# Optimization experiments

Measured on AMD Instinct MI355X. Metric: run time of the kernel, lower is better.

## Reference

```python
import jax, jax.numpy as jnp
import numpy as np

D_MODEL = 512
D_AUX = 64
B, E = 8, 2048


def setup_inputs() -> dict:
    key = jax.random.key(0)
    ks = jax.random.split(key, 12)
    x = jax.random.normal(ks[0], (B, E, D_MODEL), dtype=jnp.float32)
    query_aux = jax.random.normal(ks[1], (B, E, D_AUX), dtype=jnp.float32)
    key_aux = jax.random.normal(ks[2], (B, E, D_AUX), dtype=jnp.float32)
    adjacency_mask = jax.random.randint(ks[3], (B, E, E), 0, 2, dtype=jnp.int32)
    merge_coefficients = jax.random.uniform(ks[4], (B, E, E), dtype=jnp.float32)
    # learned parameters of IrregularityAwareAttention (nn.Linear weights stored
    # as (out, in) in torch; we keep (in, out) for x @ W)
    s = 1.0 / np.sqrt(D_MODEL)
    Wq = jax.random.uniform(ks[5], (D_MODEL, D_MODEL), minval=-s, maxval=s, dtype=jnp.float32)
    bq = jax.random.uniform(ks[6], (D_MODEL,), minval=-s, maxval=s, dtype=jnp.float32)
    Wk = jax.random.uniform(ks[7], (D_MODEL, D_MODEL), minval=-s, maxval=s, dtype=jnp.float32)
    bk = jax.random.uniform(ks[8], (D_MODEL,), minval=-s, maxval=s, dtype=jnp.float32)
    Wv = jax.random.uniform(ks[9], (D_MODEL, D_MODEL), minval=-s, maxval=s, dtype=jnp.float32)
    bv = jax.random.uniform(ks[10], (D_MODEL,), minval=-s, maxval=s, dtype=jnp.float32)
    threshold = jnp.float32(0.5)
    return {
        "x": x, "query_aux": query_aux, "key_aux": key_aux,
        "adjacency_mask": adjacency_mask, "merge_coefficients": merge_coefficients,
        "Wq": Wq, "bq": bq, "Wk": Wk, "bk": bk, "Wv": Wv, "bv": bv,
        "threshold": threshold,
    }


def reference(x, query_aux, key_aux, adjacency_mask, merge_coefficients,
              Wq, bq, Wk, bk, Wv, bv, threshold):
    d_model = x.shape[-1]
    scale = jnp.asarray(d_model, x.dtype) ** 0.5
    q = x @ Wq + bq                      # (B, E, D)
    k = x @ Wk + bk
    v = x @ Wv + bv
    scores = jnp.einsum("bed,bfd->bef", q, k) / scale   # (B, E, E)

    aux_scale = jnp.asarray(key_aux.shape[-1], x.dtype) ** 0.5
    scores_aux = jnp.einsum("bed,bfd->bef", query_aux, key_aux) / aux_scale

    non_zero_mask = scores_aux != 0
    positive_mask = scores > threshold
    merge_mask = positive_mask & non_zero_mask
    blended = (1.0 - merge_coefficients) * scores + merge_coefficients * scores_aux
    scores = jnp.where(merge_mask, blended, scores)

    mask_value = jnp.finfo(scores.dtype).min
    scores = jnp.where(adjacency_mask == 0, mask_value, scores)

    attn = jax.nn.softmax(scores, axis=-1)
    return jnp.einsum("bef,bfd->bed", attn, v)
```

## Files before the change

### kernel.cpp

```cpp
#include <hip/hip_runtime.h>

#define E2 2048
#define DM 512

typedef __attribute__((ext_vector_type(8))) _Float16 half8;
typedef __attribute__((ext_vector_type(4))) _Float16 half4;
typedef __attribute__((ext_vector_type(8))) short short8;
typedef __attribute__((ext_vector_type(4))) short shortx4;
typedef __attribute__((ext_vector_type(4))) float floatx4;

__device__ __forceinline__ void stage_tile(const _Float16* __restrict__ g, int stride,
                                           _Float16* lds, int tid) {
  const int r0 = tid >> 2;
  const int cs = ((tid & 3) ^ (r0 & 3)) * 8;
  const int wbase = (tid >> 6) * 512;
#pragma unroll
  for (int h = 0; h < 2; ++h) {
    const _Float16* gp = g + (size_t)(h * 64 + r0) * stride + cs;
    _Float16* lp = lds + h * 2048 + wbase;
    __builtin_amdgcn_global_load_lds(
        (const __attribute__((address_space(1))) unsigned int*)gp,
        (__attribute__((address_space(3))) unsigned int*)lp, 16, 0, 0);
  }
}

__device__ __forceinline__ void stage_tile8(const _Float16* __restrict__ g, int stride,
                                            _Float16* lds, int tid) {
  const int r0 = tid >> 2;
  const int cs = ((tid & 3) ^ (r0 & 3)) * 8;
  const int wbase = (tid >> 6) * 512;
  const _Float16* gp = g + (size_t)r0 * stride + cs;
  __builtin_amdgcn_global_load_lds(
      (const __attribute__((address_space(1))) unsigned int*)gp,
      (__attribute__((address_space(3))) unsigned int*)(lds + wbase), 16, 0, 0);
}

__device__ __forceinline__ void mfma16(const _Float16* As, const _Float16* Bs,
                                       floatx4 acc[4][4], int wm, int wn, int lane) {
  const int m16 = lane & 15, quad = lane >> 4;
  const int sq = (quad ^ (m16 & 3)) * 8;
  half8 a[4];
#pragma unroll
  for (int i = 0; i < 4; ++i)
    a[i] = *(const half8*)(As + (wm * 64 + i * 16 + m16) * 32 + sq);
#pragma unroll
  for (int j = 0; j < 4; ++j) {
    const half8 b = *(const half8*)(Bs + (wn * 64 + j * 16 + m16) * 32 + sq);
#pragma unroll
    for (int i = 0; i < 4; ++i)
      acc[i][j] = __builtin_amdgcn_mfma_f32_16x16x32_f16(a[i], b, acc[i][j], 0, 0, 0);
  }
}

__device__ __forceinline__ void mfma8(const _Float16* As, const _Float16* Bs,
                                      floatx4 acc[4][2], int wm, int wn, int lane) {
  const int m16 = lane & 15, quad = lane >> 4;
  const int sq = (quad ^ (m16 & 3)) * 8;
  half8 a[4];
#pragma unroll
  for (int i = 0; i < 4; ++i)
    a[i] = *(const half8*)(As + (wm * 64 + i * 16 + m16) * 32 + sq);
#pragma unroll
  for (int j = 0; j < 2; ++j) {
    const half8 b = *(const half8*)(Bs + (wn * 32 + j * 16 + m16) * 32 + sq);
#pragma unroll
    for (int i = 0; i < 4; ++i)
      acc[i][j] = __builtin_amdgcn_mfma_f32_16x16x32_f16(a[i], b, acc[i][j], 0, 0, 0);
  }
}

__device__ __forceinline__ void mfma24(const _Float16* Ah, const _Float16* Al,
                                       const _Float16* Bh, const _Float16* Bl,
                                       floatx4 acc[4][2], int wm, int wn, int lane) {
  const int m16 = lane & 15, quad = lane >> 4;
  const int sq = (quad ^ (m16 & 3)) * 8;
  half8 ah[4], al[4];
#pragma unroll
  for (int i = 0; i < 4; ++i) {
    const int off = (wm * 64 + i * 16 + m16) * 32 + sq;
    ah[i] = *(const half8*)(Ah + off);
    al[i] = *(const half8*)(Al + off);
  }
#pragma unroll
  for (int j = 0; j < 2; ++j) {
    const int off = (wn * 32 + j * 16 + m16) * 32 + sq;
    const half8 bh = *(const half8*)(Bh + off);
    const half8 bl = *(const half8*)(Bl + off);
#pragma unroll
    for (int i = 0; i < 4; ++i) {
      acc[i][j] = __builtin_amdgcn_mfma_f32_16x16x32_f16(ah[i], bh, acc[i][j], 0, 0, 0);
      acc[i][j] = __builtin_amdgcn_mfma_f32_16x16x32_f16(al[i], bh, acc[i][j], 0, 0, 0);
      acc[i][j] = __builtin_amdgcn_mfma_f32_16x16x32_f16(ah[i], bl, acc[i][j], 0, 0, 0);
    }
  }
}

__global__ void split_conv_k(const float* __restrict__ src, _Float16* __restrict__ hi,
                             _Float16* __restrict__ lo, float scale, int n8) {
  int i = blockIdx.x * blockDim.x + threadIdx.x;
  const int stride = gridDim.x * blockDim.x;
  const float4* s4 = (const float4*)src;
  for (; i < n8; i += stride) {
    const float4 u = s4[2 * i], v = s4[2 * i + 1];
    const float g[8] = {u.x, u.y, u.z, u.w, v.x, v.y, v.z, v.w};
    half8 h, l;
#pragma unroll
    for (int t = 0; t < 8; ++t) {
      const float gv = g[t] * scale;
      const _Float16 hv = (_Float16)gv;
      h[t] = hv;
      l[t] = (_Float16)(gv - (float)hv);
    }
    ((half8*)hi)[i] = h;
    ((half8*)lo)[i] = l;
  }
}

__global__ void conv_k(const float* __restrict__ src, _Float16* __restrict__ dst, int n8) {
  int i = blockIdx.x * blockDim.x + threadIdx.x;
  const int stride = gridDim.x * blockDim.x;
  const float4* s4 = (const float4*)src;
  for (; i < n8; i += stride) {
    const float4 u = s4[2 * i], v = s4[2 * i + 1];
    const float g[8] = {u.x, u.y, u.z, u.w, v.x, v.y, v.z, v.w};
    half8 h;
#pragma unroll
    for (int t = 0; t < 8; ++t) h[t] = (_Float16)g[t];
    ((half8*)dst)[i] = h;
  }
}

__global__ void transw_k(const float* __restrict__ Wq, const float* __restrict__ Wk,
                         const float* __restrict__ Wv, _Float16* __restrict__ Wth,
                         _Float16* __restrict__ Wtl) {
  const int z = blockIdx.z;
  const float* W = (z == 0) ? Wq : (z == 1) ? Wk : Wv;
  __shared__ float t[32][33];
  const int n0 = blockIdx.x * 32, k0 = blockIdx.y * 32;
  const int tx = threadIdx.x, ty = threadIdx.y;
#pragma unroll
  for (int i = 0; i < 32; i += 8) t[ty + i][tx] = W[(size_t)(k0 + ty + i) * DM + n0 + tx];
  __syncthreads();
  const size_t zb = (size_t)z * DM * DM;
#pragma unroll
  for (int i = 0; i < 32; i += 8) {
    const float g = t[tx][ty + i] * 64.0f;
    const _Float16 h = (_Float16)g;
    const size_t o = zb + (size_t)(n0 + ty + i) * DM + (k0 + tx);
    Wth[o] = h;
    Wtl[o] = (_Float16)(g - (float)h);
  }
}

__global__ __launch_bounds__(512, 4) void qkv_k(
    const _Float16* __restrict__ xh, const _Float16* __restrict__ xl,
    const _Float16* __restrict__ Wth, const _Float16* __restrict__ Wtl,
    const float* __restrict__ bqp, const float* __restrict__ bkp,
    const float* __restrict__ bvp,
    _Float16* __restrict__ qh, _Float16* __restrict__ ql,
    _Float16* __restrict__ kh, _Float16* __restrict__ kl,
    _Float16* __restrict__ vT) {
  __shared__ _Float16 Ah[2][4096], Al[2][4096], Bh[2][4096], Bl[2][4096];
  const int tid = threadIdx.x, lane = tid & 63, wv = tid >> 6;
  const int wm = wv >> 2, wn = wv & 3;
  const int bm = blockIdx.x, bn = blockIdx.y, z = blockIdx.z;
  const bool split = (z < 2);
  const _Float16* Ash = xh + (size_t)bm * 128 * DM;
  const _Float16* Asl = xl + (size_t)bm * 128 * DM;
  const _Float16* Bsh = Wth + ((size_t)z * DM + bn * 128) * DM;
  const _Float16* Bsl = Wtl + ((size_t)z * DM + bn * 128) * DM;
  floatx4 acc[4][2];
  const floatx4 z4 = {0.f, 0.f, 0.f, 0.f};
#pragma unroll
  for (int i = 0; i < 4; ++i)
#pragma unroll
    for (int j = 0; j < 2; ++j) acc[i][j] = z4;

  stage_tile8(Ash, DM, Ah[0], tid);
  stage_tile8(Bsh, DM, Bh[0], tid);
  if (split) { stage_tile8(Asl, DM, Al[0], tid); stage_tile8(Bsl, DM, Bl[0], tid); }
  __syncthreads();
  for (int kt = 0; kt < 16; ++kt) {
    const int cur = kt & 1, nxt = cur ^ 1;
    if (kt < 15) {
      const int ko = (kt + 1) * 32;
      stage_tile8(Ash + ko, DM, Ah[nxt], tid);
      stage_tile8(Bsh + ko, DM, Bh[nxt], tid);
      if (split) { stage_tile8(Asl + ko, DM, Al[nxt], tid); stage_tile8(Bsl + ko, DM, Bl[nxt], tid); }
    }
    if (split) mfma24(Ah[cur], Al[cur], Bh[cur], Bl[cur], acc, wm, wn, lane);
    else       mfma8(Ah[cur], Bh[cur], acc, wm, wn, lane);
    __syncthreads();
  }
  const int m16 = lane & 15, quad = lane >> 4;
  const float* bias = (z == 0) ? bqp : (z == 1) ? bkp : bvp;
  if (split) {
    _Float16* oh = (z == 0) ? qh : kh;
    _Float16* ol = (z == 0) ? ql : kl;
#pragma unroll
    for (int j = 0; j < 2; ++j) {
      const int n = bn * 128 + wn * 32 + j * 16 + m16;
      const float bb = bias[n];
#pragma unroll
      for (int i = 0; i < 4; ++i) {
        const int m = bm * 128 + wm * 64 + i * 16 + quad * 4;
#pragma unroll
        for (int r = 0; r < 4; ++r) {
          const float val = acc[i][j][r] * (1.0f / 256.0f) + bb;
          const float v8 = val * 8.0f;
          const _Float16 h = (_Float16)v8;
          const _Float16 l = (_Float16)(v8 - (float)h);
          const size_t o = (size_t)(m + r) * DM + n;
          oh[o] = h; ol[o] = l;
        }
      }
    }
  } else {
#pragma unroll
    for (int j = 0; j < 2; ++j) {
      const int n = bn * 128 + wn * 32 + j * 16 + m16;
      const float bb = bias[n];
#pragma unroll
      for (int i = 0; i < 4; ++i) {
        const int m = bm * 128 + wm * 64 + i * 16 + quad * 4;
        const int bidx = m >> 11, e0 = m & 2047;
        half4 pk;
#pragma unroll
        for (int r = 0; r < 4; ++r)
          pk[r] = (_Float16)(acc[i][j][r] * (1.0f / 256.0f) + bb);
        *(half4*)(vT + ((size_t)bidx * DM + n) * E2 + e0) = pk;
      }
    }
  }
}

__global__ __launch_bounds__(512, 4) void scores_k(
    const _Float16* __restrict__ qh, const _Float16* __restrict__ ql,
    const _Float16* __restrict__ kh, const _Float16* __restrict__ kl,
    const _Float16* __restrict__ qah, const _Float16* __restrict__ kah,
    const float* __restrict__ mc,
    const float* __restrict__ thrp, unsigned short* __restrict__ sc) {
  __shared__ _Float16 S[32768];
  _Float16* const AhB = S;
  _Float16* const AlB = S + 8192;
  _Float16* const BhB = S + 16384;
  _Float16* const BlB = S + 24576;
  const int tid = threadIdx.x, lane = tid & 63, wv = tid >> 6;
  const int wm = wv >> 2, wn = wv & 3;
  const int bf = blockIdx.x, be = blockIdx.y, b = blockIdx.z;
  const _Float16* Ash = qh + ((size_t)b * E2 + be * 128) * DM;
  const _Float16* Asl = ql + ((size_t)b * E2 + be * 128) * DM;
  const _Float16* Bsh = kh + ((size_t)b * E2 + bf * 128) * DM;
  const _Float16* Bsl = kl + ((size_t)b * E2 + bf * 128) * DM;
  floatx4 accm[4][2];
  const floatx4 z4 = {0.f, 0.f, 0.f, 0.f};
#pragma unroll
  for (int i = 0; i < 4; ++i)
#pragma unroll
    for (int j = 0; j < 2; ++j) accm[i][j] = z4;

  stage_tile8(Ash, DM, AhB, tid);
  stage_tile8(Bsh, DM, BhB, tid);
  stage_tile8(Asl, DM, AlB, tid);
  stage_tile8(Bsl, DM, BlB, tid);
  __syncthreads();
  for (int kt = 0; kt < 16; ++kt) {
    const int cur = kt & 1, nxt = cur ^ 1;
    if (kt < 15) {
      const int ko = (kt + 1) * 32;
      stage_tile8(Ash + ko, DM, AhB + nxt * 4096, tid);
      stage_tile8(Bsh + ko, DM, BhB + nxt * 4096, tid);
      stage_tile8(Asl + ko, DM, AlB + nxt * 4096, tid);
      stage_tile8(Bsl + ko, DM, BlB + nxt * 4096, tid);
    }
    mfma24(AhB + cur * 4096, AlB + cur * 4096, BhB + cur * 4096, BlB + cur * 4096,
           accm, wm, wn, lane);
    __syncthreads();
  }
  floatx4 acca[4][2];
#pragma unroll
  for (int i = 0; i < 4; ++i)
#pragma unroll
    for (int j = 0; j < 2; ++j) acca[i][j] = z4;
  const _Float16* A2 = qah + ((size_t)b * E2 + be * 128) * 64;
  const _Float16* B2 = kah + ((size_t)b * E2 + bf * 128) * 64;
  stage_tile8(A2, 64, AhB, tid);
  stage_tile8(B2, 64, BhB, tid);
  stage_tile8(A2 + 32, 64, AhB + 4096, tid);
  stage_tile8(B2 + 32, 64, BhB + 4096, tid);
  __syncthreads();
  mfma8(AhB, BhB, acca, wm, wn, lane);
  mfma8(AhB + 4096, BhB + 4096, acca, wm, wn, lane);

  float* const sL = (float*)S;
  _Float16* const saL = S + 16896;
  const float thr = *thrp;
  const int m16 = lane & 15, quad = lane >> 4;
  const size_t rowbase0 = (size_t)b * E2 + be * 128;
#pragma unroll
  for (int h = 0; h < 2; ++h) {
    __syncthreads();
    if (wm == h) {
#pragma unroll
      for (int j = 0; j < 2; ++j) {
        const int cl = wn * 32 + j * 16 + m16;
#pragma unroll
        for (int i = 0; i < 4; ++i) {
#pragma unroll
          for (int r = 0; r < 4; ++r) {
            const int rl = i * 16 + quad * 4 + r;
            sL[rl * 132 + cl] = accm[i][j][r] * (0.015625f * 0.044194173824159216f);
            saL[rl * 132 + cl] = (_Float16)(acca[i][j][r] * 0.125f);
          }
        }
      }
    }
    __syncthreads();
#pragma unroll
    for (int g = 0; g < 4; ++g) {
      const int tf = g * 2048 + tid * 4;
      const int rl = tf >> 7, cl = tf & 127;
      const size_t idx = (rowbase0 + h * 64 + rl) * E2 + bf * 128 + cl;
      const float4 c4 = *(const float4*)(mc + idx);
      const float4 s4v = *(const float4*)(sL + rl * 132 + cl);
      const half4 sa4 = *(const half4*)(saL + rl * 132 + cl);
      const float ss[4] = {s4v.x, s4v.y, s4v.z, s4v.w};
      const float cc[4] = {c4.x, c4.y, c4.z, c4.w};
      shortx4 o;
#pragma unroll
      for (int t = 0; t < 4; ++t) {
        float s = ss[t];
        const float sa = (float)sa4[t];
        if (sa != 0.0f && s > thr) s = (1.0f - cc[t]) * s + cc[t] * sa;
        union { _Float16 hh; unsigned short u; } u;
        u.hh = (_Float16)s;
        o[t] = (short)u.u;
      }
      *(shortx4*)(sc + idx) = o;
    }
  }
}

__global__ __launch_bounds__(256) void smax_k(unsigned short* __restrict__ sc,
                                              const int* __restrict__ adj) {
  const size_t row = blockIdx.x;
  unsigned short* p = sc + row * E2;
  const int* arow = adj + row * E2;
  const int tid = threadIdx.x, lane = tid & 63, wv = tid >> 6;
  const short8 raw = *(const short8*)(p + tid * 8);
  const int4 a0 = *(const int4*)(arow + tid * 8);
  const int4 a1 = *(const int4*)(arow + tid * 8 + 4);
  const int aa[8] = {a0.x, a0.y, a0.z, a0.w, a1.x, a1.y, a1.z, a1.w};
  float f[8];
#pragma unroll
  for (int t = 0; t < 8; ++t) {
    union { _Float16 h; short s; } u; u.s = raw[t];
    f[t] = aa[t] ? (float)u.h : -65504.0f;
  }
  float mx = f[0];
#pragma unroll
  for (int t = 1; t < 8; ++t) mx = fmaxf(mx, f[t]);
#pragma unroll
  for (int o = 32; o > 0; o >>= 1) mx = fmaxf(mx, __shfl_xor(mx, o, 64));
  __shared__ float red[8];
  if (lane == 0) red[wv] = mx;
  __syncthreads();
  mx = fmaxf(fmaxf(red[0], red[1]), fmaxf(red[2], red[3]));
  float ef[8], sum = 0.f;
#pragma unroll
  for (int t = 0; t < 8; ++t) { ef[t] = __expf(f[t] - mx); sum += ef[t]; }
#pragma unroll
  for (int o = 32; o > 0; o >>= 1) sum += __shfl_xor(sum, o, 64);
  if (lane == 0) red[4 + wv] = sum;
  __syncthreads();
  sum = (red[4] + red[5]) + (red[6] + red[7]);
  const float inv = 1.0f / sum;
  short8 ov;
#pragma unroll
  for (int t = 0; t < 8; ++t) {
    union { _Float16 h; short s; } u;
    u.h = (_Float16)(ef[t] * inv);
    ov[t] = u.s;
  }
  *(short8*)(p + tid * 8) = ov;
}

__global__ __launch_bounds__(256, 2) void pv_k(
    const _Float16* __restrict__ at, const _Float16* __restrict__ vT,
    float* __restrict__ out) {
  __shared__ _Float16 As[2][4096], Bs[2][4096];
  const int tid = threadIdx.x, lane = tid & 63, wv = tid >> 6;
  const int wm = wv >> 1, wn = wv & 1;
  const int bd = blockIdx.x, be = blockIdx.y, b = blockIdx.z;
  const _Float16* Asrc = at + ((size_t)b * E2 + be * 128) * E2;
  const _Float16* Bsrc = vT + ((size_t)b * DM + bd * 128) * E2;
  floatx4 acc[4][4];
  const floatx4 z4 = {0.f, 0.f, 0.f, 0.f};
#pragma unroll
  for (int i = 0; i < 4; ++i)
#pragma unroll
    for (int j = 0; j < 4; ++j) acc[i][j] = z4;
  stage_tile(Asrc, E2, As[0], tid);
  stage_tile(Bsrc, E2, Bs[0], tid);
  __syncthreads();
  for (int kt = 0; kt < 64; ++kt) {
    const int cur = kt & 1, nxt = cur ^ 1;
    if (kt < 63) {
      const int ko = (kt + 1) * 32;
      stage_tile(Asrc + ko, E2, As[nxt], tid);
      stage_tile(Bsrc + ko, E2, Bs[nxt], tid);
    }
    mfma16(As[cur], Bs[cur], acc, wm, wn, lane);
    __syncthreads();
  }
  const int m16 = lane & 15, quad = lane >> 4;
#pragma unroll
  for (int j = 0; j < 4; ++j) {
    const int d = bd * 128 + wn * 64 + j * 16 + m16;
#pragma unroll
    for (int i = 0; i < 4; ++i) {
      const int e0 = be * 128 + wm * 64 + i * 16 + quad * 4;
#pragma unroll
      for (int r = 0; r < 4; ++r)
        out[((size_t)b * E2 + e0 + r) * DM + d] = acc[i][j][r];
    }
  }
}

extern "C" void kernel_launch(void* const* d_in, const int* in_sizes, int n_in,
                              void* d_out, int out_size, void* d_ws, size_t ws_size,
                              hipStream_t stream) {
  const float* x   = (const float*)d_in[0];
  const float* qa  = (const float*)d_in[1];
  const float* ka  = (const float*)d_in[2];
  const int*   adj = (const int*)d_in[3];
  const float* mc  = (const float*)d_in[4];
  const float* Wq  = (const float*)d_in[5];
  const float* bq  = (const float*)d_in[6];
  const float* Wk  = (const float*)d_in[7];
  const float* bk  = (const float*)d_in[8];
  const float* Wv  = (const float*)d_in[9];
  const float* bv  = (const float*)d_in[10];
  const float* thr = (const float*)d_in[11];
  float* out = (float*)d_out;
  char* w = (char*)d_ws;
  const size_t MiB = 1ull << 20;
  _Float16* xh  = (_Float16*)(w + 0 * MiB);
  _Float16* xl  = (_Float16*)(w + 16 * MiB);
  _Float16* qhp = (_Float16*)(w + 32 * MiB);
  _Float16* qlp = (_Float16*)(w + 48 * MiB);
  _Float16* khp = (_Float16*)(w + 64 * MiB);
  _Float16* klp = (_Float16*)(w + 80 * MiB);
  _Float16* vT  = (_Float16*)(w + 96 * MiB);
  _Float16* Wth = (_Float16*)(w + 112 * MiB);
  _Float16* Wtl = (_Float16*)(w + 114 * MiB);
  _Float16* qah = (_Float16*)(w + 116 * MiB);
  _Float16* kah = (_Float16*)(w + 118 * MiB);
  unsigned short* sc = (unsigned short*)(w + 120 * MiB);

  split_conv_k<<<2048, 256, 0, stream>>>(x, xh, xl, 4.0f, (8 * E2 * DM) / 8);
  conv_k<<<256, 256, 0, stream>>>(qa, qah, (8 * E2 * 64) / 8);
  conv_k<<<256, 256, 0, stream>>>(ka, kah, (8 * E2 * 64) / 8);
  transw_k<<<dim3(16, 16, 3), dim3(32, 8), 0, stream>>>(Wq, Wk, Wv, Wth, Wtl);
  qkv_k<<<dim3(128, 4, 3), 512, 0, stream>>>(xh, xl, Wth, Wtl, bq, bk, bv,
                                             qhp, qlp, khp, klp, vT);
  scores_k<<<dim3(16, 16, 8), 512, 0, stream>>>(qhp, qlp, khp, klp, qah, kah,
                                                mc, thr, sc);
  smax_k<<<16384, 256, 0, stream>>>(sc, adj);
  pv_k<<<dim3(4, 16, 8), 256, 0, stream>>>((const _Float16*)sc, vT, out);
}
```

Measured before the change: 583.0 us.

## Remap block IDs for XCD locality and widen pv_k to 512 threads

Remaps the linear block index in qkv_k, scores_k and pv_k so that blocks landing on the same XCD (round-robin by 8) work on contiguous tiles sharing the same batch and operands. The aim is better L2 reuse on the multi-die MI355X. pv_k also moves from 4 waves with 64x64 warp tiles to 8 waves with 64x32 warp tiles per block, using single-load staging. This raises occupancy and cuts per-wave register pressure, at the cost of more LDS reads per MFMA.

```diff
diff --git a/kernel.cpp b/kernel.cpp
--- a/kernel.cpp
+++ b/kernel.cpp
@@ -8,21 +8,6 @@
 typedef __attribute__((ext_vector_type(8))) short short8;
 typedef __attribute__((ext_vector_type(4))) short shortx4;
 typedef __attribute__((ext_vector_type(4))) float floatx4;
-
-__device__ __forceinline__ void stage_tile(const _Float16* __restrict__ g, int stride,
-                                           _Float16* lds, int tid) {
-  const int r0 = tid >> 2;
-  const int cs = ((tid & 3) ^ (r0 & 3)) * 8;
-  const int wbase = (tid >> 6) * 512;
-#pragma unroll
-  for (int h = 0; h < 2; ++h) {
-    const _Float16* gp = g + (size_t)(h * 64 + r0) * stride + cs;
-    _Float16* lp = lds + h * 2048 + wbase;
-    __builtin_amdgcn_global_load_lds(
-        (const __attribute__((address_space(1))) unsigned int*)gp,
-        (__attribute__((address_space(3))) unsigned int*)lp, 16, 0, 0);
-  }
-}
 
 __device__ __forceinline__ void stage_tile8(const _Float16* __restrict__ g, int stride,
                                             _Float16* lds, int tid) {
@@ -33,23 +18,6 @@
   __builtin_amdgcn_global_load_lds(
       (const __attribute__((address_space(1))) unsigned int*)gp,
       (__attribute__((address_space(3))) unsigned int*)(lds + wbase), 16, 0, 0);
-}
-
-__device__ __forceinline__ void mfma16(const _Float16* As, const _Float16* Bs,
-                                       floatx4 acc[4][4], int wm, int wn, int lane) {
-  const int m16 = lane & 15, quad = lane >> 4;
-  const int sq = (quad ^ (m16 & 3)) * 8;
-  half8 a[4];
-#pragma unroll
-  for (int i = 0; i < 4; ++i)
-    a[i] = *(const half8*)(As + (wm * 64 + i * 16 + m16) * 32 + sq);
-#pragma unroll
-  for (int j = 0; j < 4; ++j) {
-    const half8 b = *(const half8*)(Bs + (wn * 64 + j * 16 + m16) * 32 + sq);
-#pragma unroll
-    for (int i = 0; i < 4; ++i)
-      acc[i][j] = __builtin_amdgcn_mfma_f32_16x16x32_f16(a[i], b, acc[i][j], 0, 0, 0);
-  }
 }
 
 __device__ __forceinline__ void mfma8(const _Float16* As, const _Float16* Bs,
@@ -163,7 +131,9 @@
   __shared__ _Float16 Ah[2][4096], Al[2][4096], Bh[2][4096], Bl[2][4096];
   const int tid = threadIdx.x, lane = tid & 63, wv = tid >> 6;
   const int wm = wv >> 2, wn = wv & 3;
-  const int bm = blockIdx.x, bn = blockIdx.y, z = blockIdx.z;
+  const int flat = blockIdx.x + 128 * blockIdx.y + 512 * blockIdx.z;
+  const int virt = (flat & 7) * 192 + (flat >> 3);
+  const int bm = virt & 127, bn = (virt >> 7) & 3, z = virt >> 9;
   const bool split = (z < 2);
   const _Float16* Ash = xh + (size_t)bm * 128 * DM;
   const _Float16* Asl = xl + (size_t)bm * 128 * DM;
@@ -247,7 +217,9 @@
   _Float16* const BlB = S + 24576;
   const int tid = threadIdx.x, lane = tid & 63, wv = tid >> 6;
   const int wm = wv >> 2, wn = wv & 3;
-  const int bf = blockIdx.x, be = blockIdx.y, b = blockIdx.z;
+  const int flat = blockIdx.x + 16 * blockIdx.y + 256 * blockIdx.z;
+  const int virt = (flat & 7) * 256 + (flat >> 3);
+  const int bf = virt & 15, be = (virt >> 4) & 15, b = virt >> 8;
   const _Float16* Ash = qh + ((size_t)b * E2 + be * 128) * DM;
   const _Float16* Asl = ql + ((size_t)b * E2 + be * 128) * DM;
   const _Float16* Bsh = kh + ((size_t)b * E2 + bf * 128) * DM;
@@ -385,38 +357,40 @@
   *(short8*)(p + tid * 8) = ov;
 }
 
-__global__ __launch_bounds__(256, 2) void pv_k(
+__global__ __launch_bounds__(512, 6) void pv_k(
     const _Float16* __restrict__ at, const _Float16* __restrict__ vT,
     float* __restrict__ out) {
   __shared__ _Float16 As[2][4096], Bs[2][4096];
   const int tid = threadIdx.x, lane = tid & 63, wv = tid >> 6;
-  const int wm = wv >> 1, wn = wv & 1;
-  const int bd = blockIdx.x, be = blockIdx.y, b = blockIdx.z;
+  const int wm = wv >> 2, wn = wv & 3;
+  const int flat = blockIdx.x + 4 * blockIdx.y + 64 * blockIdx.z;
+  const int virt = (flat & 7) * 64 + (flat >> 3);
+  const int bd = virt & 3, be = (virt >> 2) & 15, b = virt >> 6;
   const _Float16* Asrc = at + ((size_t)b * E2 + be * 128) * E2;
   const _Float16* Bsrc = vT + ((size_t)b * DM + bd * 128) * E2;
-  floatx4 acc[4][4];
+  floatx4 acc[4][2];
   const floatx4 z4 = {0.f, 0.f, 0.f, 0.f};
 #pragma unroll
   for (int i = 0; i < 4; ++i)
 #pragma unroll
-    for (int j = 0; j < 4; ++j) acc[i][j] = z4;
-  stage_tile(Asrc, E2, As[0], tid);
-  stage_tile(Bsrc, E2, Bs[0], tid);
+    for (int j = 0; j < 2; ++j) acc[i][j] = z4;
+  stage_tile8(Asrc, E2, As[0], tid);
+  stage_tile8(Bsrc, E2, Bs[0], tid);
   __syncthreads();
   for (int kt = 0; kt < 64; ++kt) {
     const int cur = kt & 1, nxt = cur ^ 1;
     if (kt < 63) {
       const int ko = (kt + 1) * 32;
-      stage_tile(Asrc + ko, E2, As[nxt], tid);
-      stage_tile(Bsrc + ko, E2, Bs[nxt], tid);
-    }
-    mfma16(As[cur], Bs[cur], acc, wm, wn, lane);
+      stage_tile8(Asrc + ko, E2, As[nxt], tid);
+      stage_tile8(Bsrc + ko, E2, Bs[nxt], tid);
+    }
+    mfma8(As[cur], Bs[cur], acc, wm, wn, lane);
     __syncthreads();
   }
   const int m16 = lane & 15, quad = lane >> 4;
 #pragma unroll
-  for (int j = 0; j < 4; ++j) {
-    const int d = bd * 128 + wn * 64 + j * 16 + m16;
+  for (int j = 0; j < 2; ++j) {
+    const int d = bd * 128 + wn * 32 + j * 16 + m16;
 #pragma unroll
     for (int i = 0; i < 4; ++i) {
       const int e0 = be * 128 + wm * 64 + i * 16 + quad * 4;
@@ -467,5 +441,5 @@
   scores_k<<<dim3(16, 16, 8), 512, 0, stream>>>(qhp, qlp, khp, klp, qah, kah,
                                                 mc, thr, sc);
   smax_k<<<16384, 256, 0, stream>>>(sc, adj);
-  pv_k<<<dim3(4, 16, 8), 256, 0, stream>>>((const _Float16*)sc, vT, out);
-}
+  pv_k<<<dim3(4, 16, 8), 512, 0, stream>>>((const _Float16*)sc, vT, out);
+}
```

Measured after the change: 589.9 us. No clear change (+1.2%).
